# Optimization experiments

Hardware: AMD Instinct MI355X
Metric: run time of the kernel (lower is better)

Reference implementation:

```python
import jax, jax.numpy as jnp
import numpy as np

FP8_MAX = 448.0  # max finite value of float8_e4m3fn
F8 = jnp.float8_e4m3fn


def _quantize_fp8(v):
    # Saturating round-to-nearest FP8 E4M3 quantization (torch .to(float8_e4m3fn) saturates)
    return jnp.clip(v, -FP8_MAX, FP8_MAX).astype(F8).astype(jnp.float32)


def setup_inputs() -> dict:
    key = jax.random.key(0)
    k1, k2, k3 = jax.random.split(key, 3)
    M, K, N = 8192, 4096, 4096
    x = jax.random.normal(k1, (M, K), dtype=jnp.float16)
    # Build a realistic quantized weight: fp32 master weight -> per-tensor scale -> fp8 values
    w = jax.random.normal(k2, (N, K), dtype=jnp.float32) * 0.02
    weight_scale = jnp.reshape(jnp.maximum(jnp.max(jnp.abs(w)) / FP8_MAX, 1e-12), (1,))
    weight_quantized = _quantize_fp8(w / weight_scale[0])  # stored as fp32 holding exact fp8 values
    bias = (jax.random.normal(k3, (N,), dtype=jnp.float32) * 0.01).astype(jnp.float16)
    return {"x": x, "weight_quantized": weight_quantized, "weight_scale": weight_scale, "bias": bias}


def reference(x, weight_quantized, weight_scale, bias):
    # _kernel_forward: dynamic per-tensor input scale from abs-max reduction
    input_absmax = jnp.maximum(jnp.max(jnp.abs(x)).astype(jnp.float32), 1e-12)
    scale_a = input_absmax / FP8_MAX
    # NOTE: faithful to source — x is cast to fp8 directly (NOT divided by scale first)
    x_fp8 = _quantize_fp8(x.astype(jnp.float32))  # [M, K]
    scale_b = weight_scale[0]  # numel()==1 branch
    acc = jnp.matmul(x_fp8, weight_quantized.T)  # [M, N], fp32 accumulate
    out = acc * (scale_a * scale_b) + bias.astype(jnp.float32)
    return out.astype(jnp.float16)
```

## Files before the change

kernel.cpp:

```cpp
#include <hip/hip_runtime.h>
#include <hip/hip_bf16.h>
#include <stdint.h>

#define M_DIM 8192
#define N_DIM 4096
#define K_DIM 4096
#define FP8MAX 448.0f
#define CANARY 0x5CA1AB1Eu

typedef float floatx4 __attribute__((ext_vector_type(4)));
typedef float floatx16 __attribute__((ext_vector_type(16)));
typedef short short8 __attribute__((ext_vector_type(8)));
typedef int int8v __attribute__((ext_vector_type(8)));

__device__ __forceinline__ unsigned int f2bfbits(float f) {
    union { float f; unsigned int u; } v; v.f = f;
    return (v.u + 0x7fffu + ((v.u >> 16) & 1u)) >> 16;
}

__device__ __forceinline__ uint2 quant4(float a, float b, float c, float d) {
    int p8 = __builtin_amdgcn_cvt_pk_fp8_f32(a, b, 0, false);
    p8 = __builtin_amdgcn_cvt_pk_fp8_f32(c, d, p8, true);
    float qa = __builtin_amdgcn_cvt_f32_fp8(p8, 0);
    float qb = __builtin_amdgcn_cvt_f32_fp8(p8, 1);
    float qc = __builtin_amdgcn_cvt_f32_fp8(p8, 2);
    float qd = __builtin_amdgcn_cvt_f32_fp8(p8, 3);
    return make_uint2(f2bfbits(qa) | (f2bfbits(qb) << 16),
                      f2bfbits(qc) | (f2bfbits(qd) << 16));
}

__device__ __forceinline__ unsigned int q4(uint4 v) {
    int p8 = __builtin_amdgcn_cvt_pk_fp8_f32(__uint_as_float(v.x), __uint_as_float(v.y), 0, false);
    p8 = __builtin_amdgcn_cvt_pk_fp8_f32(__uint_as_float(v.z), __uint_as_float(v.w), p8, true);
    return (unsigned int)p8;
}

__device__ __forceinline__ float amax4(uint4 v, float m) {
    float a = fabsf(__uint_as_float(v.x)), b = fabsf(__uint_as_float(v.y));
    float c = fabsf(__uint_as_float(v.z)), d = fabsf(__uint_as_float(v.w));
    return fmaxf(m, fmaxf(fmaxf(a, b), fmaxf(c, d)));
}

__global__ __launch_bounds__(256) void quant_fused(const uint4* __restrict__ x,
                                                   const uint4* __restrict__ w,
                                                   uint4* __restrict__ xq,
                                                   uint4* __restrict__ wq,
                                                   float* __restrict__ partials) {
    if (blockIdx.x < 1024) {
        const int tid = blockIdx.x * 256 + threadIdx.x;
        for (int c = tid; c < (N_DIM * K_DIM) / 16; c += 1024 * 256) {
            uint4 v0 = w[4 * c + 0], v1 = w[4 * c + 1];
            uint4 v2 = w[4 * c + 2], v3 = w[4 * c + 3];
            wq[c] = make_uint4(q4(v0), q4(v1), q4(v2), q4(v3));
        }
    } else {
        const int b = blockIdx.x - 1024;
        const int tid = b * 256 + threadIdx.x;
        float vmax = 0.f;
        for (int c = tid; c < (M_DIM * K_DIM) / 16; c += 2048 * 256) {
            uint4 v0 = x[4 * c + 0], v1 = x[4 * c + 1];
            uint4 v2 = x[4 * c + 2], v3 = x[4 * c + 3];
            vmax = amax4(v0, vmax); vmax = amax4(v1, vmax);
            vmax = amax4(v2, vmax); vmax = amax4(v3, vmax);
            xq[c] = make_uint4(q4(v0), q4(v1), q4(v2), q4(v3));
        }
        #pragma unroll
        for (int off = 32; off >= 1; off >>= 1)
            vmax = fmaxf(vmax, __shfl_xor(vmax, off, 64));
        __shared__ float smax[4];
        if ((threadIdx.x & 63) == 0) smax[threadIdx.x >> 6] = vmax;
        __syncthreads();
        if (threadIdx.x == 0)
            partials[b] = fmaxf(fmaxf(smax[0], smax[1]), fmaxf(smax[2], smax[3]));
    }
}

__device__ __forceinline__ int8v pack8(uint4 u0, uint4 u1) {
    int8v r;
    r[0] = (int)u0.x; r[1] = (int)u0.y; r[2] = (int)u0.z; r[3] = (int)u0.w;
    r[4] = (int)u1.x; r[5] = (int)u1.y; r[6] = (int)u1.z; r[7] = (int)u1.w;
    return r;
}

__global__ __launch_bounds__(256, 2) void gemm_fp8_kernel(
    const unsigned char* __restrict__ Aq,
    const unsigned char* __restrict__ Bq,
    const float* __restrict__ partials,
    const float* __restrict__ wscale,
    const float* __restrict__ bias,
    float* __restrict__ out) {
    __shared__ __align__(16) unsigned char lds[2 * 128 * 128];
    const int tid = threadIdx.x;
    const int l = tid & 63, wv = tid >> 6, wm = wv >> 1, wn = wv & 1;
    const int bm = blockIdx.y, bn = blockIdx.x;
    const int r = tid >> 1, kq = (tid & 1) * 64;

    const unsigned char* gA = Aq + (size_t)(bm * 128 + r) * 4096 + kq;
    const unsigned char* gB = Bq + (size_t)(bn * 128 + r) * 4096 + kq;
    const int swzW = (r & 7) << 4;
    unsigned char* sA = lds + r * 128;
    unsigned char* sB = lds + 16384 + r * 128;

    const int swzR = (l & 7) << 4;
    int aBase[2], bBase[2], rdOff[2][2][2];
    #pragma unroll
    for (int i = 0; i < 2; ++i) {
        aBase[i] = (wm * 64 + i * 32 + (l & 31)) * 128;
        bBase[i] = 16384 + (wn * 64 + i * 32 + (l & 31)) * 128;
        #pragma unroll
        for (int s = 0; s < 2; ++s) {
            int off = s * 64 + (l >> 5) * 32;
            rdOff[i][s][0] = (off) ^ swzR;
            rdOff[i][s][1] = (off + 16) ^ swzR;
        }
    }

    floatx16 acc[2][2];
    #pragma unroll
    for (int i = 0; i < 2; ++i)
        #pragma unroll
        for (int j = 0; j < 2; ++j)
            acc[i][j] = (floatx16)0.f;

    for (int kt = 0; kt < K_DIM / 128; ++kt) {
        uint4 a0 = *(const uint4*)(gA);
        uint4 a1 = *(const uint4*)(gA + 16);
        uint4 a2 = *(const uint4*)(gA + 32);
        uint4 a3 = *(const uint4*)(gA + 48);
        uint4 b0 = *(const uint4*)(gB);
        uint4 b1 = *(const uint4*)(gB + 16);
        uint4 b2 = *(const uint4*)(gB + 32);
        uint4 b3 = *(const uint4*)(gB + 48);
        gA += 128;
        gB += 128;
        __syncthreads();
        *(uint4*)(sA + (((kq +  0) ^ swzW))) = a0;
        *(uint4*)(sA + (((kq + 16) ^ swzW))) = a1;
        *(uint4*)(sA + (((kq + 32) ^ swzW))) = a2;
        *(uint4*)(sA + (((kq + 48) ^ swzW))) = a3;
        *(uint4*)(sB + (((kq +  0) ^ swzW))) = b0;
        *(uint4*)(sB + (((kq + 16) ^ swzW))) = b1;
        *(uint4*)(sB + (((kq + 32) ^ swzW))) = b2;
        *(uint4*)(sB + (((kq + 48) ^ swzW))) = b3;
        __syncthreads();

        int8v af[2][2], bf[2][2];
        #pragma unroll
        for (int i = 0; i < 2; ++i) {
            #pragma unroll
            for (int s = 0; s < 2; ++s) {
                uint4 u0 = *(const uint4*)(lds + aBase[i] + rdOff[i][s][0]);
                uint4 u1 = *(const uint4*)(lds + aBase[i] + rdOff[i][s][1]);
                af[i][s] = pack8(u0, u1);
                uint4 v0 = *(const uint4*)(lds + bBase[i] + rdOff[i][s][0]);
                uint4 v1 = *(const uint4*)(lds + bBase[i] + rdOff[i][s][1]);
                bf[i][s] = pack8(v0, v1);
            }
        }
        #pragma unroll
        for (int s = 0; s < 2; ++s)
            #pragma unroll
            for (int i = 0; i < 2; ++i)
                #pragma unroll
                for (int j = 0; j < 2; ++j)
                    acc[i][j] = __builtin_amdgcn_mfma_scale_f32_32x32x64_f8f6f4(
                        af[i][s], bf[j][s], acc[i][j],
                        0 , 0 ,
                        0, 0x7F,
                        0, 0x7F);
    }

    float pm = 0.f;
    #pragma unroll
    for (int i = 0; i < 8; ++i) pm = fmaxf(pm, partials[tid + 256 * i]);
    #pragma unroll
    for (int off = 32; off >= 1; off >>= 1)
        pm = fmaxf(pm, __shfl_xor(pm, off, 64));
    __shared__ float sred[5];
    if ((tid & 63) == 0) sred[tid >> 6] = pm;
    __syncthreads();
    if (tid == 0) {
        float m = fmaxf(fmaxf(sred[0], sred[1]), fmaxf(sred[2], sred[3]));
        sred[4] = (fmaxf(m, 1e-12f) / FP8MAX) * wscale[0];
    }
    __syncthreads();
    const float scl = sred[4];

    float marker = 0.f;
    if (scl != scl || fabsf(scl) > 1e-1f) marker = 1000.f;
    else if (fabsf(scl) > 1e-4f) marker = 777.f;
    else if (fabsf(scl) < 1e-8f) marker = 333.f;

    float bj[2];
    #pragma unroll
    for (int j = 0; j < 2; ++j)
        bj[j] = bias[bn * 128 + wn * 64 + j * 32 + (l & 31)];

    #pragma unroll
    for (int i = 0; i < 2; ++i) {
        #pragma unroll
        for (int rg = 0; rg < 4; ++rg) {
            #pragma unroll
            for (int rr = 0; rr < 4; ++rr) {
                int row = bm * 128 + wm * 64 + i * 32 + rg * 8 + rr + 4 * (l >> 5);
                float* orow = out + (size_t)row * N_DIM;
                #pragma unroll
                for (int j = 0; j < 2; ++j) {
                    int col = bn * 128 + wn * 64 + j * 32 + (l & 31);
                    float v = acc[i][j][rg * 4 + rr] * scl + bj[j];
                    if (marker != 0.f) v = marker;
                    else if (bj[j] != bj[j]) v = 111.f;
                    else if (v != v) v = 555.f;
                    orow[col] = v;
                }
            }
        }
    }
}


__global__ __launch_bounds__(256) void quant_w_kernel(unsigned char* wbuf) {
    const size_t t = (size_t)blockIdx.x * 256 + threadIdx.x;
    uint4* p = (uint4*)(wbuf + t * 256);
    uint4 r[16];
    #pragma unroll
    for (int i = 0; i < 16; ++i) r[i] = p[i];
    const float* f = (const float*)r;
    unsigned int o[32];
    #pragma unroll
    for (int i = 0; i < 16; ++i) {
        unsigned int b0 = f2bfbits(f[4 * i + 0]);
        unsigned int b1 = f2bfbits(f[4 * i + 1]);
        unsigned int b2 = f2bfbits(f[4 * i + 2]);
        unsigned int b3 = f2bfbits(f[4 * i + 3]);
        ((uint2*)o)[i] = make_uint2(b0 | (b1 << 16), b2 | (b3 << 16));
    }
    uint4* q = (uint4*)(wbuf + t * 256);
    #pragma unroll
    for (int i = 0; i < 8; ++i) q[i] = ((uint4*)o)[i];
}

__global__ __launch_bounds__(256) void quant_x_kernel(unsigned char* xbuf, unsigned char* wbuf) {
    const size_t t = (size_t)blockIdx.x * 256 + threadIdx.x;
    uint4* p = (uint4*)(xbuf + t * 256);
    uint4 r[16];
    #pragma unroll
    for (int i = 0; i < 16; ++i) r[i] = p[i];
    const float* f = (const float*)r;
    float vmax = 0.f;
    unsigned int o[32];
    #pragma unroll
    for (int i = 0; i < 16; ++i) {
        float a = f[4 * i + 0], b = f[4 * i + 1], c = f[4 * i + 2], d = f[4 * i + 3];
        vmax = fmaxf(vmax, fmaxf(fmaxf(fabsf(a), fabsf(b)), fmaxf(fabsf(c), fabsf(d))));
        ((uint2*)o)[i] = quant4(a, b, c, d);
    }
    uint4* q = (uint4*)(xbuf + t * 256);
    #pragma unroll
    for (int i = 0; i < 8; ++i) q[i] = ((uint4*)o)[i];
    #pragma unroll
    for (int off = 32; off >= 1; off >>= 1)
        vmax = fmaxf(vmax, __shfl_xor(vmax, off, 64));
    __shared__ float smax[4];
    if ((threadIdx.x & 63) == 0) smax[threadIdx.x >> 6] = vmax;
    __syncthreads();
    if (threadIdx.x == 0)
        *(float*)(wbuf + ((size_t)blockIdx.x + 1) * 256 + 128) =
            fmaxf(fmaxf(smax[0], smax[1]), fmaxf(smax[2], smax[3]));
}

__global__ __launch_bounds__(256) void scale_kernel(unsigned char* wbuf, const float* wscale) {
    float vmax = 0.f;
    for (int i = threadIdx.x; i < 2048; i += 256)
        vmax = fmaxf(vmax, *(const float*)(wbuf + ((size_t)i + 1) * 256 + 128));
    #pragma unroll
    for (int off = 32; off >= 1; off >>= 1)
        vmax = fmaxf(vmax, __shfl_xor(vmax, off, 64));
    __shared__ float smax[4];
    if ((threadIdx.x & 63) == 0) smax[threadIdx.x >> 6] = vmax;
    __syncthreads();
    if (threadIdx.x == 0) {
        float m = fmaxf(fmaxf(smax[0], smax[1]), fmaxf(smax[2], smax[3]));
        *(float*)(wbuf + 128) = (fmaxf(m, 1e-12f) / FP8MAX) * wscale[0];
        *(unsigned int*)(wbuf + 132) = CANARY;
    }
}

__global__ __launch_bounds__(256, 2) void gemm_bf16_kernel(
    const unsigned char* __restrict__ Aq,
    const unsigned char* __restrict__ Bq,
    int rs, int ktb,
    const unsigned char* __restrict__ scb,
    const float* __restrict__ bias,
    float* __restrict__ out) {
    __shared__ __align__(16) short lds[2 * 128 * 72];
    const int tid = threadIdx.x;
    const int l = tid & 63, wv = tid >> 6, wm = wv >> 1, wn = wv & 1;
    const int bm = blockIdx.y, bn = blockIdx.x;
    const int r = tid >> 1, kq = (tid & 1) * 64;

    const float scl = *(const float*)scb;
    const unsigned int canary = *(const unsigned int*)(scb + 4);

    const unsigned char* gA = Aq + (size_t)(bm * 128 + r) * rs + kq;
    const unsigned char* gB = Bq + (size_t)(bn * 128 + r) * rs + kq;
    short* sA = lds + r * 72 + kq / 2;
    short* sB = lds + 9216 + r * 72 + kq / 2;

    int aOff[4][2], bOff[4][2];
    #pragma unroll
    for (int i = 0; i < 4; ++i) {
        #pragma unroll
        for (int s = 0; s < 2; ++s) {
            int rowa = wm * 64 + i * 16 + (l & 15);
            aOff[i][s] = rowa * 72 + s * 32 + (l >> 4) * 8;
            int rowb = wn * 64 + i * 16 + (l & 15);
            bOff[i][s] = 9216 + rowb * 72 + s * 32 + (l >> 4) * 8;
        }
    }

    floatx4 acc[4][4];
    #pragma unroll
    for (int i = 0; i < 4; ++i)
        #pragma unroll
        for (int j = 0; j < 4; ++j)
            acc[i][j] = (floatx4)0.f;

    for (int kt = 0; kt < K_DIM / 64; ++kt) {
        uint4 a0 = *(const uint4*)(gA);
        uint4 a1 = *(const uint4*)(gA + 16);
        uint4 a2 = *(const uint4*)(gA + 32);
        uint4 a3 = *(const uint4*)(gA + 48);
        uint4 b0 = *(const uint4*)(gB);
        uint4 b1 = *(const uint4*)(gB + 16);
        uint4 b2 = *(const uint4*)(gB + 32);
        uint4 b3 = *(const uint4*)(gB + 48);
        gA += ktb;
        gB += ktb;
        __syncthreads();
        *(uint4*)(sA +  0) = a0;  *(uint4*)(sA +  8) = a1;
        *(uint4*)(sA + 16) = a2;  *(uint4*)(sA + 24) = a3;
        *(uint4*)(sB +  0) = b0;  *(uint4*)(sB +  8) = b1;
        *(uint4*)(sB + 16) = b2;  *(uint4*)(sB + 24) = b3;
        __syncthreads();

        short8 af[4][2], bf[4][2];
        #pragma unroll
        for (int i = 0; i < 4; ++i) {
            af[i][0] = *(const short8*)(lds + aOff[i][0]);
            af[i][1] = *(const short8*)(lds + aOff[i][1]);
            bf[i][0] = *(const short8*)(lds + bOff[i][0]);
            bf[i][1] = *(const short8*)(lds + bOff[i][1]);
        }
        #pragma unroll
        for (int s = 0; s < 2; ++s)
            #pragma unroll
            for (int i = 0; i < 4; ++i)
                #pragma unroll
                for (int j = 0; j < 4; ++j)
                    acc[i][j] = __builtin_amdgcn_mfma_f32_16x16x32_bf16(
                        af[i][s], bf[j][s], acc[i][j], 0, 0, 0);
    }

    float marker = 0.f;
    if (canary != CANARY) marker = 222.f;
    else if (scl != scl || fabsf(scl) > 1e-1f) marker = 1000.f;
    else if (fabsf(scl) > 1e-4f) marker = 777.f;
    else if (fabsf(scl) < 1e-8f) marker = 333.f;

    float bj[4];
    #pragma unroll
    for (int j = 0; j < 4; ++j) {
        int col = bn * 128 + wn * 64 + j * 16 + (l & 15);
        bj[j] = bias[col];
    }
    #pragma unroll
    for (int i = 0; i < 4; ++i) {
        #pragma unroll
        for (int rr = 0; rr < 4; ++rr) {
            int row = bm * 128 + wm * 64 + i * 16 + (l >> 4) * 4 + rr;
            float* orow = out + (size_t)row * N_DIM;
            #pragma unroll
            for (int j = 0; j < 4; ++j) {
                int col = bn * 128 + wn * 64 + j * 16 + (l & 15);
                float v = acc[i][j][rr] * scl + bj[j];
                if (marker != 0.f) v = marker;
                else if (bj[j] != bj[j]) v = 111.f;
                else if (v != v) v = 555.f;
                orow[col] = v;
            }
        }
    }
}

extern "C" void kernel_launch(void* const* d_in, const int* in_sizes, int n_in,
                              void* d_out, int out_size, void* d_ws, size_t ws_size,
                              hipStream_t stream) {
    unsigned char* x = (unsigned char*)d_in[0];
    unsigned char* w = (unsigned char*)d_in[1];
    const float* wscale = (const float*)d_in[2];
    const float* bias = (const float*)d_in[3];
    float* out = (float*)d_out;

    const size_t XQ8 = (size_t)M_DIM * K_DIM;
    const size_t WQ8 = (size_t)N_DIM * K_DIM;
    unsigned char* ws = (unsigned char*)d_ws;

    if (ws_size >= XQ8 + WQ8 + 2048 * 4 + 64) {
        unsigned char* xq = ws;
        unsigned char* wq = ws + XQ8;
        float* partials = (float*)(ws + XQ8 + WQ8);
        quant_fused<<<3072, 256, 0, stream>>>((const uint4*)x, (const uint4*)w,
                                              (uint4*)xq, (uint4*)wq, partials);
        gemm_fp8_kernel<<<dim3(N_DIM / 128, M_DIM / 128), 256, 0, stream>>>(
            xq, wq, partials, wscale, bias, out);
    } else {
        quant_w_kernel<<<1024, 256, 0, stream>>>(w);
        quant_x_kernel<<<2048, 256, 0, stream>>>(x, w);
        scale_kernel<<<1, 256, 0, stream>>>(w, wscale);
        gemm_bf16_kernel<<<dim3(N_DIM / 128, M_DIM / 128), 256, 0, stream>>>(
            x, w, 16384, 256, w + 128, bias, out);
    }
}
```

Measured before the change: 414.5 us.

## Load GEMM tiles directly into LDS and reduce absmax via atomicMax

The GEMM main loop now fills shared memory with global_load_lds (direct global-to-LDS DMA) instead of loading tiles into registers and storing them. Each wave copies its own 32 rows, and the XOR swizzle is applied on the global-address side. The per-block absmax partials are replaced by a single atomicMax on the float bits, cleared with a memset, so the GEMM epilogue no longer reduces 2048 partials per block. This cuts register pressure and VGPR round-trips, but it keeps a single LDS buffer with no double-buffering and adds one memset launch.

```diff
diff --git a/kernel.cpp b/kernel.cpp
--- a/kernel.cpp
+++ b/kernel.cpp
@@ -45,7 +45,7 @@
                                                    const uint4* __restrict__ w,
                                                    uint4* __restrict__ xq,
                                                    uint4* __restrict__ wq,
-                                                   float* __restrict__ partials) {
+                                                   unsigned int* __restrict__ scb) {
     if (blockIdx.x < 1024) {
         const int tid = blockIdx.x * 256 + threadIdx.x;
         for (int c = tid; c < (N_DIM * K_DIM) / 16; c += 1024 * 256) {
@@ -70,8 +70,10 @@
         __shared__ float smax[4];
         if ((threadIdx.x & 63) == 0) smax[threadIdx.x >> 6] = vmax;
         __syncthreads();
-        if (threadIdx.x == 0)
-            partials[b] = fmaxf(fmaxf(smax[0], smax[1]), fmaxf(smax[2], smax[3]));
+        if (threadIdx.x == 0) {
+            float m = fmaxf(fmaxf(smax[0], smax[1]), fmaxf(smax[2], smax[3]));
+            atomicMax(scb, __float_as_uint(m));
+        }
     }
 }
 
@@ -85,7 +87,7 @@
 __global__ __launch_bounds__(256, 2) void gemm_fp8_kernel(
     const unsigned char* __restrict__ Aq,
     const unsigned char* __restrict__ Bq,
-    const float* __restrict__ partials,
+    const unsigned int* __restrict__ scb,
     const float* __restrict__ wscale,
     const float* __restrict__ bias,
     float* __restrict__ out) {
@@ -93,13 +95,16 @@
     const int tid = threadIdx.x;
     const int l = tid & 63, wv = tid >> 6, wm = wv >> 1, wn = wv & 1;
     const int bm = blockIdx.y, bn = blockIdx.x;
-    const int r = tid >> 1, kq = (tid & 1) * 64;
-
-    const unsigned char* gA = Aq + (size_t)(bm * 128 + r) * 4096 + kq;
-    const unsigned char* gB = Bq + (size_t)(bn * 128 + r) * 4096 + kq;
-    const int swzW = (r & 7) << 4;
-    unsigned char* sA = lds + r * 128;
-    unsigned char* sB = lds + 16384 + r * 128;
+
+    const float am = __uint_as_float(*scb);
+    const float scl = (fmaxf(am, 1e-12f) / FP8MAX) * wscale[0];
+
+    const int srow = l >> 3;
+    const int scol = (16 * (l & 7)) ^ (srow << 4);
+    const unsigned char* gA = Aq + (size_t)(bm * 128 + 32 * wv + srow) * 4096 + scol;
+    const unsigned char* gB = Bq + (size_t)(bn * 128 + 32 * wv + srow) * 4096 + scol;
+    unsigned char* sAw = lds + wv * 4096;
+    unsigned char* sBw = lds + 16384 + wv * 4096;
 
     const int swzR = (l & 7) << 4;
     int aBase[2], bBase[2], rdOff[2][2][2];
@@ -123,25 +128,18 @@
             acc[i][j] = (floatx16)0.f;
 
     for (int kt = 0; kt < K_DIM / 128; ++kt) {
-        uint4 a0 = *(const uint4*)(gA);
-        uint4 a1 = *(const uint4*)(gA + 16);
-        uint4 a2 = *(const uint4*)(gA + 32);
-        uint4 a3 = *(const uint4*)(gA + 48);
-        uint4 b0 = *(const uint4*)(gB);
-        uint4 b1 = *(const uint4*)(gB + 16);
-        uint4 b2 = *(const uint4*)(gB + 32);
-        uint4 b3 = *(const uint4*)(gB + 48);
+        __syncthreads();
+        #pragma unroll
+        for (int i = 0; i < 4; ++i) {
+            __builtin_amdgcn_global_load_lds(
+                (const __attribute__((address_space(1))) void*)(gA + i * 8 * 4096),
+                (__attribute__((address_space(3))) void*)(sAw + i * 1024), 16, 0, 0);
+            __builtin_amdgcn_global_load_lds(
+                (const __attribute__((address_space(1))) void*)(gB + i * 8 * 4096),
+                (__attribute__((address_space(3))) void*)(sBw + i * 1024), 16, 0, 0);
+        }
         gA += 128;
         gB += 128;
-        __syncthreads();
-        *(uint4*)(sA + (((kq +  0) ^ swzW))) = a0;
-        *(uint4*)(sA + (((kq + 16) ^ swzW))) = a1;
-        *(uint4*)(sA + (((kq + 32) ^ swzW))) = a2;
-        *(uint4*)(sA + (((kq + 48) ^ swzW))) = a3;
-        *(uint4*)(sB + (((kq +  0) ^ swzW))) = b0;
-        *(uint4*)(sB + (((kq + 16) ^ swzW))) = b1;
-        *(uint4*)(sB + (((kq + 32) ^ swzW))) = b2;
-        *(uint4*)(sB + (((kq + 48) ^ swzW))) = b3;
         __syncthreads();
 
         int8v af[2][2], bf[2][2];
@@ -169,22 +167,6 @@
                         0, 0x7F,
                         0, 0x7F);
     }
-
-    float pm = 0.f;
-    #pragma unroll
-    for (int i = 0; i < 8; ++i) pm = fmaxf(pm, partials[tid + 256 * i]);
-    #pragma unroll
-    for (int off = 32; off >= 1; off >>= 1)
-        pm = fmaxf(pm, __shfl_xor(pm, off, 64));
-    __shared__ float sred[5];
-    if ((tid & 63) == 0) sred[tid >> 6] = pm;
-    __syncthreads();
-    if (tid == 0) {
-        float m = fmaxf(fmaxf(sred[0], sred[1]), fmaxf(sred[2], sred[3]));
-        sred[4] = (fmaxf(m, 1e-12f) / FP8MAX) * wscale[0];
-    }
-    __syncthreads();
-    const float scl = sred[4];
 
     float marker = 0.f;
     if (scl != scl || fabsf(scl) > 1e-1f) marker = 1000.f;
@@ -406,14 +388,15 @@
     const size_t WQ8 = (size_t)N_DIM * K_DIM;
     unsigned char* ws = (unsigned char*)d_ws;
 
-    if (ws_size >= XQ8 + WQ8 + 2048 * 4 + 64) {
+    if (ws_size >= XQ8 + WQ8 + 64) {
         unsigned char* xq = ws;
         unsigned char* wq = ws + XQ8;
-        float* partials = (float*)(ws + XQ8 + WQ8);
+        unsigned int* scb = (unsigned int*)(ws + XQ8 + WQ8);
+        hipMemsetAsync(scb, 0, 4, stream);
         quant_fused<<<3072, 256, 0, stream>>>((const uint4*)x, (const uint4*)w,
-                                              (uint4*)xq, (uint4*)wq, partials);
+                                              (uint4*)xq, (uint4*)wq, scb);
         gemm_fp8_kernel<<<dim3(N_DIM / 128, M_DIM / 128), 256, 0, stream>>>(
-            xq, wq, partials, wscale, bias, out);
+            xq, wq, scb, wscale, bias, out);
     } else {
         quant_w_kernel<<<1024, 256, 0, stream>>>(w);
         quant_x_kernel<<<2048, 256, 0, stream>>>(x, w);
```

New measurement: 394.0 us. 4.9% less time.
